# Kernel optimization log

Measured on AMD Instinct MI355X. Metric: run time of the kernel, lower is better.

## Reference

```python
import jax, jax.numpy as jnp
import numpy as np

NOISE_STD = 0.1
TOP_K = 2


def setup_inputs() -> dict:
    key = jax.random.key(0)
    k_x, k_n, k_w, k_keys = jax.random.split(key, 4)
    N, D_IN, D_Q, K = 16384, 2048, 256, 64
    x = jax.random.normal(k_x, (N, D_IN), dtype=jnp.float32)
    noise = jax.random.normal(k_n, (N, K), dtype=jnp.float32)
    # Linear params (kaiming-uniform-ish scale) and xavier-uniform keys
    w_q = jax.random.normal(k_w, (D_IN, D_Q), dtype=jnp.float32) * (1.0 / np.sqrt(D_IN))
    b_q = jnp.zeros((D_Q,), dtype=jnp.float32)
    lim = np.sqrt(6.0 / (K + D_Q))
    keys = jax.random.uniform(k_keys, (K, D_Q), dtype=jnp.float32, minval=-lim, maxval=lim)
    return {"x": x, "noise": noise, "w_q": w_q, "b_q": b_q, "keys": keys}


def reference(x, noise, w_q, b_q, keys):
    # query projection: [N, D_in] @ [D_in, D_q] -> [N, D_q]
    query = x @ w_q + b_q
    d_q = query.shape[-1]
    # router logits: [N, K], scaled dot product with expert keys
    logits = (query @ keys.T) * (1.0 / jnp.sqrt(jnp.asarray(d_q, query.dtype)))
    logits = logits + noise * NOISE_STD  # training-mode gating noise
    # top-k selection + softmax over selected logits only
    top_logits, top_idx = jax.lax.top_k(logits, TOP_K)       # [N, top_k]
    top_probs = jax.nn.softmax(top_logits, axis=-1)           # [N, top_k]
    # scatter selected probs into dense [N, K] gating tensor (zeros elsewhere)
    rows = jnp.arange(logits.shape[0])[:, None]               # [N, 1]
    gating_probs = jnp.zeros_like(logits).at[rows, top_idx].set(top_probs)
    return gating_probs, top_idx
```

## Files before the change

kernel.cpp:

```cpp
#include <hip/hip_runtime.h>

#define MROWS 16384
#define KD 2048
#define NQ 256
#define NE 64
#define INV_SQRT_DQ 0.0625f
#define NOISE_STD_C 0.1f

typedef _Float16 f16x8 __attribute__((ext_vector_type(8)));
typedef float f32x4 __attribute__((ext_vector_type(4)));

__device__ inline void split8v(f32x4 a, f32x4 b, f16x8* h, f16x8* l) {
    f16x8 hh, ll;
#pragma unroll
    for (int i = 0; i < 4; ++i) {
        _Float16 s = (_Float16)a[i];
        hh[i] = s; ll[i] = (_Float16)(a[i] - (float)s);
    }
#pragma unroll
    for (int i = 0; i < 4; ++i) {
        _Float16 s = (_Float16)b[i];
        hh[4 + i] = s; ll[4 + i] = (_Float16)(b[i] - (float)s);
    }
    *h = hh; *l = ll;
}

__global__ __launch_bounds__(256) void prep_w2(
    const float* __restrict__ w, const float* __restrict__ keys,
    const float* __restrict__ bq, _Float16* __restrict__ whp,
    _Float16* __restrict__ wlp, float* __restrict__ css) {
    const int tid = blockIdx.x * 256 + threadIdx.x;
    const int e = tid & 63;
    const int o = tid >> 6;
    const float* kp = keys + (size_t)e * NQ;
    const float* wp = w + (size_t)o * 8 * NQ;
    double acc[8];
#pragma unroll
    for (int j = 0; j < 8; ++j) acc[j] = 0.0;
    for (int q = 0; q < NQ; q += 4) {
        f32x4 kv = *(const f32x4*)(kp + q);
#pragma unroll
        for (int j = 0; j < 8; ++j) {
            f32x4 wv = *(const f32x4*)(wp + (size_t)j * NQ + q);
#pragma unroll
            for (int u = 0; u < 4; ++u)
                acc[j] += (double)wv[u] * (double)kv[u];
        }
    }
    const int kc32 = o >> 2;
    const int qqp  = o & 3;
    const size_t base = ((size_t)kc32 * 4 + (e >> 4)) * 512 + (size_t)(qqp * 16 + (e & 15)) * 8;
    f16x8 h, l;
#pragma unroll
    for (int j = 0; j < 8; ++j) {
        float v = (float)acc[j];
        _Float16 s = (_Float16)v;
        h[j] = s;
        l[j] = (_Float16)(v - (float)s);
    }
    *(f16x8*)(whp + base) = h;
    *(f16x8*)(wlp + base) = l;
    if (blockIdx.x == 0 && threadIdx.x < NE) {
        const float* kp2 = keys + (size_t)threadIdx.x * NQ;
        double s = 0.0;
        for (int q = 0; q < NQ; ++q) s += (double)bq[q] * (double)kp2[q];
        css[threadIdx.x] = (float)(s * 0.0625);
    }
}

__global__ __launch_bounds__(512) void gemm2_fused(
    const float* __restrict__ x, const _Float16* __restrict__ whp,
    const _Float16* __restrict__ wlp, const float* __restrict__ css,
    const float* __restrict__ noise, float* __restrict__ gate,
    float* __restrict__ idxout) {
    __shared__ __align__(16) char smem[65536];

    const int t = threadIdx.x;
    const int lane = t & 63;
    const int wv = t >> 6;
    const int wn = wv & 3;
    const int wm = wv >> 2;
    const int m0 = blockIdx.x * 64;
    const int f = lane & 15;
    const int qq = lane >> 4;

    const int srow = t >> 4;
    const int soct = t & 15;
    const int swoff = (soct ^ (srow & 7)) * 8;
    const f32x4* xq0 = (const f32x4*)(x + (size_t)(m0 + srow) * KD + soct * 8);
    const f32x4* xq1 = (const f32x4*)(x + (size_t)(m0 + srow + 32) * KD + soct * 8);

    const _Float16* bph = whp + (size_t)wn * 512 + lane * 8;
    const _Float16* bpl = wlp + (size_t)wn * 512 + lane * 8;

    f32x4 acc[2];
    acc[0] = {0.f, 0.f, 0.f, 0.f};
    acc[1] = {0.f, 0.f, 0.f, 0.f};

    f32x4 a0 = __builtin_nontemporal_load(xq0);
    f32x4 a1 = __builtin_nontemporal_load(xq0 + 1);
    f32x4 b0 = __builtin_nontemporal_load(xq1);
    f32x4 b1 = __builtin_nontemporal_load(xq1 + 1);
    {
        _Float16* Ah = (_Float16*)smem;
        _Float16* Al = Ah + 8192;
        f16x8 h8, l8;
        split8v(a0, a1, &h8, &l8);
        *(f16x8*)(Ah + srow * 128 + swoff) = h8;
        *(f16x8*)(Al + srow * 128 + swoff) = l8;
        split8v(b0, b1, &h8, &l8);
        *(f16x8*)(Ah + (srow + 32) * 128 + swoff) = h8;
        *(f16x8*)(Al + (srow + 32) * 128 + swoff) = l8;
    }
    a0 = __builtin_nontemporal_load(xq0 + 32);
    a1 = __builtin_nontemporal_load(xq0 + 33);
    b0 = __builtin_nontemporal_load(xq1 + 32);
    b1 = __builtin_nontemporal_load(xq1 + 33);
    __syncthreads();

    f16x8 bhS[4], blS[4];
#pragma unroll
    for (int ks = 0; ks < 4; ++ks) {
        bhS[ks] = *(const f16x8*)(bph + (size_t)ks * 2048);
        blS[ks] = *(const f16x8*)(bpl + (size_t)ks * 2048);
    }

    for (int i = 0; i < 16; ++i) {
        _Float16* AhC = (_Float16*)smem + (i & 1) * 16384;
        _Float16* AlC = AhC + 8192;
        _Float16* AhN = (_Float16*)smem + ((i & 1) ^ 1) * 16384;
        _Float16* AlN = AhN + 8192;

        if (i < 15) {
            f16x8 h8, l8;
            split8v(a0, a1, &h8, &l8);
            *(f16x8*)(AhN + srow * 128 + swoff) = h8;
            *(f16x8*)(AlN + srow * 128 + swoff) = l8;
            split8v(b0, b1, &h8, &l8);
            *(f16x8*)(AhN + (srow + 32) * 128 + swoff) = h8;
            *(f16x8*)(AlN + (srow + 32) * 128 + swoff) = l8;
        }
        if (i < 14) {
            a0 = __builtin_nontemporal_load(xq0 + (i + 2) * 32);
            a1 = __builtin_nontemporal_load(xq0 + (i + 2) * 32 + 1);
            b0 = __builtin_nontemporal_load(xq1 + (i + 2) * 32);
            b1 = __builtin_nontemporal_load(xq1 + (i + 2) * 32 + 1);
        }
#pragma unroll
        for (int ks = 0; ks < 4; ++ks) {
            f16x8 ah[2], al[2];
#pragma unroll
            for (int mt = 0; mt < 2; ++mt) {
                const int row = (wm * 2 + mt) * 16 + f;
                const int ab = row * 128 + (((ks * 4 + qq) ^ (row & 7)) * 8);
                ah[mt] = *(const f16x8*)(AhC + ab);
                al[mt] = *(const f16x8*)(AlC + ab);
            }
#pragma unroll
            for (int mt = 0; mt < 2; ++mt) {
                acc[mt] = __builtin_amdgcn_mfma_f32_16x16x32_f16(ah[mt], bhS[ks], acc[mt], 0, 0, 0);
                acc[mt] = __builtin_amdgcn_mfma_f32_16x16x32_f16(ah[mt], blS[ks], acc[mt], 0, 0, 0);
                acc[mt] = __builtin_amdgcn_mfma_f32_16x16x32_f16(al[mt], bhS[ks], acc[mt], 0, 0, 0);
            }
            int gn = i * 4 + ks + 4;
            if (gn > 63) gn = 63;
            bhS[ks] = *(const f16x8*)(bph + (size_t)gn * 2048);
            blS[ks] = *(const f16x8*)(bpl + (size_t)gn * 2048);
        }
        asm volatile("" ::: "memory");
        __builtin_amdgcn_s_waitcnt(0xC07F);
        __builtin_amdgcn_s_barrier();
        asm volatile("" ::: "memory");
    }

    float* LG = (float*)smem;
    const int e = wn * 16 + f;
    const float cse = css[e];
#pragma unroll
    for (int mt = 0; mt < 2; ++mt)
#pragma unroll
        for (int r = 0; r < 4; ++r) {
            int row = (wm * 2 + mt) * 16 + qq * 4 + r;
            LG[row * 65 + e] = acc[mt][r] * INV_SQRT_DQ + cse +
                               NOISE_STD_C * noise[(size_t)(m0 + row) * NE + e];
        }
    __syncthreads();

    for (int i = 0; i < 8; ++i) {
        int r = wv * 8 + i;
        float v = LG[r * 65 + lane];
        float v1 = v; int i1 = lane;
#pragma unroll
        for (int off = 32; off; off >>= 1) {
            float ov = __shfl_xor(v1, off);
            int oi = __shfl_xor(i1, off);
            if (ov > v1 || (ov == v1 && oi < i1)) { v1 = ov; i1 = oi; }
        }
        float v2 = (lane == i1) ? -1e30f : v;
        int i2 = lane;
#pragma unroll
        for (int off = 32; off; off >>= 1) {
            float ov = __shfl_xor(v2, off);
            int oi = __shfl_xor(i2, off);
            if (ov > v2 || (ov == v2 && oi < i2)) { v2 = ov; i2 = oi; }
        }
        float ex = expf(v2 - v1);
        float p1 = 1.0f / (1.0f + ex);
        float p2 = ex * p1;
        float g = (lane == i1) ? p1 : ((lane == i2) ? p2 : 0.0f);
        gate[(size_t)(m0 + r) * NE + lane] = g;
        if (lane == 0) {
            float2 ii = make_float2((float)i1, (float)i2);
            *(float2*)(idxout + (size_t)(m0 + r) * 2) = ii;
        }
    }
}

extern "C" void kernel_launch(void* const* d_in, const int* in_sizes, int n_in,
                              void* d_out, int out_size, void* d_ws, size_t ws_size,
                              hipStream_t stream) {
    const float* x     = (const float*)d_in[0];
    const float* noise = (const float*)d_in[1];
    const float* w_q   = (const float*)d_in[2];
    const float* b_q   = (const float*)d_in[3];
    const float* keys  = (const float*)d_in[4];
    float* out = (float*)d_out;

    char* ws = (char*)d_ws;
    _Float16* whp = (_Float16*)ws;
    _Float16* wlp = (_Float16*)(ws + (256u << 10));
    float* css    = (float*)(ws + (512u << 10));

    prep_w2<<<64, 256, 0, stream>>>(w_q, keys, b_q, whp, wlp, css);
    gemm2_fused<<<256, 512, 0, stream>>>(x, whp, wlp, css, noise,
                                         out, out + (size_t)MROWS * NE);
}
```

Baseline: 252.4 us.

## Split-K GEMM with 16-row blocks and register-direct x loads, parallelize prep

The main kernel moves from 64-row tiles staged through double-buffered LDS to 16-row blocks. Each of 4 waves handles a quarter of K, loads x straight into registers, and a wave-0 reduction through shared memory combines the partial sums. This drops the per-iteration LDS staging and barriers and raises the grid from 256 to 1024 blocks at 2 blocks per CU. The prep kernel also splits its dot products across 4 threads with a shared-memory reduction, so it can run on more blocks. In exchange, each wave now fetches the full fused weight matrix instead of sharing it, which raises L2 traffic for the weights.

```diff
diff --git a/kernel.cpp b/kernel.cpp
--- a/kernel.cpp
+++ b/kernel.cpp
@@ -29,15 +29,17 @@
     const float* __restrict__ w, const float* __restrict__ keys,
     const float* __restrict__ bq, _Float16* __restrict__ whp,
     _Float16* __restrict__ wlp, float* __restrict__ css) {
-    const int tid = blockIdx.x * 256 + threadIdx.x;
-    const int e = tid & 63;
-    const int o = tid >> 6;
-    const float* kp = keys + (size_t)e * NQ;
-    const float* wp = w + (size_t)o * 8 * NQ;
+    __shared__ double part[4][64][8];
+    const int t = threadIdx.x;
+    const int e = t & 63;
+    const int qc = t >> 6;
+    const int o = blockIdx.x;
+    const float* kp = keys + (size_t)e * NQ + qc * 64;
+    const float* wp = w + (size_t)o * 8 * NQ + qc * 64;
     double acc[8];
 #pragma unroll
     for (int j = 0; j < 8; ++j) acc[j] = 0.0;
-    for (int q = 0; q < NQ; q += 4) {
+    for (int q = 0; q < 64; q += 4) {
         f32x4 kv = *(const f32x4*)(kp + q);
 #pragma unroll
         for (int j = 0; j < 8; ++j) {
@@ -47,147 +49,144 @@
                 acc[j] += (double)wv[u] * (double)kv[u];
         }
     }
-    const int kc32 = o >> 2;
-    const int qqp  = o & 3;
-    const size_t base = ((size_t)kc32 * 4 + (e >> 4)) * 512 + (size_t)(qqp * 16 + (e & 15)) * 8;
-    f16x8 h, l;
-#pragma unroll
-    for (int j = 0; j < 8; ++j) {
-        float v = (float)acc[j];
-        _Float16 s = (_Float16)v;
-        h[j] = s;
-        l[j] = (_Float16)(v - (float)s);
-    }
-    *(f16x8*)(whp + base) = h;
-    *(f16x8*)(wlp + base) = l;
-    if (blockIdx.x == 0 && threadIdx.x < NE) {
-        const float* kp2 = keys + (size_t)threadIdx.x * NQ;
-        double s = 0.0;
-        for (int q = 0; q < NQ; ++q) s += (double)bq[q] * (double)kp2[q];
-        css[threadIdx.x] = (float)(s * 0.0625);
-    }
-}
-
-__global__ __launch_bounds__(512) void gemm2_fused(
+#pragma unroll
+    for (int j = 0; j < 8; ++j) part[qc][e][j] = acc[j];
+    __syncthreads();
+    if (t < 64) {
+        const size_t base = ((size_t)(o >> 2) * 4 + (e >> 4)) * 512 +
+                            (size_t)((o & 3) * 16 + (e & 15)) * 8;
+        f16x8 h, l;
+#pragma unroll
+        for (int j = 0; j < 8; ++j) {
+            float v = (float)(part[0][e][j] + part[1][e][j] +
+                              part[2][e][j] + part[3][e][j]);
+            _Float16 s = (_Float16)v;
+            h[j] = s;
+            l[j] = (_Float16)(v - (float)s);
+        }
+        *(f16x8*)(whp + base) = h;
+        *(f16x8*)(wlp + base) = l;
+    }
+    if (blockIdx.x == 0) {
+        __syncthreads();
+        double p = 0.0;
+        const float* bp2 = bq + qc * 64;
+        const float* kp2 = keys + (size_t)e * NQ + qc * 64;
+        for (int q = 0; q < 64; q += 4) {
+            f32x4 bv = *(const f32x4*)(bp2 + q);
+            f32x4 kv = *(const f32x4*)(kp2 + q);
+#pragma unroll
+            for (int u = 0; u < 4; ++u)
+                p += (double)bv[u] * (double)kv[u];
+        }
+        part[qc][e][0] = p;
+        __syncthreads();
+        if (t < 64)
+            css[e] = (float)((part[0][e][0] + part[1][e][0] +
+                              part[2][e][0] + part[3][e][0]) * 0.0625);
+    }
+}
+
+__global__ __launch_bounds__(256, 2) void gemm3_fused(
     const float* __restrict__ x, const _Float16* __restrict__ whp,
     const _Float16* __restrict__ wlp, const float* __restrict__ css,
     const float* __restrict__ noise, float* __restrict__ gate,
     float* __restrict__ idxout) {
-    __shared__ __align__(16) char smem[65536];
+    __shared__ float comb[3 * 1040];
+    __shared__ float LG[16 * 65];
 
     const int t = threadIdx.x;
     const int lane = t & 63;
     const int wv = t >> 6;
-    const int wn = wv & 3;
-    const int wm = wv >> 2;
-    const int m0 = blockIdx.x * 64;
+    const int m0 = blockIdx.x * 16;
     const int f = lane & 15;
     const int qq = lane >> 4;
 
-    const int srow = t >> 4;
-    const int soct = t & 15;
-    const int swoff = (soct ^ (srow & 7)) * 8;
-    const f32x4* xq0 = (const f32x4*)(x + (size_t)(m0 + srow) * KD + soct * 8);
-    const f32x4* xq1 = (const f32x4*)(x + (size_t)(m0 + srow + 32) * KD + soct * 8);
-
-    const _Float16* bph = whp + (size_t)wn * 512 + lane * 8;
-    const _Float16* bpl = wlp + (size_t)wn * 512 + lane * 8;
-
-    f32x4 acc[2];
-    acc[0] = {0.f, 0.f, 0.f, 0.f};
-    acc[1] = {0.f, 0.f, 0.f, 0.f};
-
-    f32x4 a0 = __builtin_nontemporal_load(xq0);
-    f32x4 a1 = __builtin_nontemporal_load(xq0 + 1);
-    f32x4 b0 = __builtin_nontemporal_load(xq1);
-    f32x4 b1 = __builtin_nontemporal_load(xq1 + 1);
-    {
-        _Float16* Ah = (_Float16*)smem;
-        _Float16* Al = Ah + 8192;
-        f16x8 h8, l8;
-        split8v(a0, a1, &h8, &l8);
-        *(f16x8*)(Ah + srow * 128 + swoff) = h8;
-        *(f16x8*)(Al + srow * 128 + swoff) = l8;
-        split8v(b0, b1, &h8, &l8);
-        *(f16x8*)(Ah + (srow + 32) * 128 + swoff) = h8;
-        *(f16x8*)(Al + (srow + 32) * 128 + swoff) = l8;
-    }
-    a0 = __builtin_nontemporal_load(xq0 + 32);
-    a1 = __builtin_nontemporal_load(xq0 + 33);
-    b0 = __builtin_nontemporal_load(xq1 + 32);
-    b1 = __builtin_nontemporal_load(xq1 + 33);
+    const float* xp = x + (size_t)(m0 + f) * KD + wv * 512 + qq * 8;
+    const _Float16* bph = whp + (size_t)(wv * 16) * 2048 + lane * 8;
+    const _Float16* bpl = wlp + (size_t)(wv * 16) * 2048 + lane * 8;
+
+    f32x4 acc[4];
+#pragma unroll
+    for (int nt = 0; nt < 4; ++nt) acc[nt] = {0.f, 0.f, 0.f, 0.f};
+
+    f32x4 xb[4][2];
+    f16x8 bhS[2][4], blS[2][4];
+
+#pragma unroll
+    for (int s = 0; s < 4; ++s) {
+        const f32x4* p = (const f32x4*)(xp + s * 32);
+        xb[s][0] = __builtin_nontemporal_load(p);
+        xb[s][1] = __builtin_nontemporal_load(p + 1);
+    }
+#pragma unroll
+    for (int s = 0; s < 2; ++s)
+#pragma unroll
+        for (int nt = 0; nt < 4; ++nt) {
+            bhS[s][nt] = *(const f16x8*)(bph + ((size_t)s * 4 + nt) * 512);
+            blS[s][nt] = *(const f16x8*)(bpl + ((size_t)s * 4 + nt) * 512);
+        }
+
+#pragma unroll
+    for (int s = 0; s < 16; ++s) {
+        const int js = s & 3;
+        const int c = s & 1;
+        f16x8 ah, al;
+        split8v(xb[js][0], xb[js][1], &ah, &al);
+#pragma unroll
+        for (int nt = 0; nt < 4; ++nt) {
+            acc[nt] = __builtin_amdgcn_mfma_f32_16x16x32_f16(ah, bhS[c][nt], acc[nt], 0, 0, 0);
+            acc[nt] = __builtin_amdgcn_mfma_f32_16x16x32_f16(ah, blS[c][nt], acc[nt], 0, 0, 0);
+            acc[nt] = __builtin_amdgcn_mfma_f32_16x16x32_f16(al, bhS[c][nt], acc[nt], 0, 0, 0);
+        }
+        if (s < 12) {
+            const f32x4* p = (const f32x4*)(xp + (s + 4) * 32);
+            xb[js][0] = __builtin_nontemporal_load(p);
+            xb[js][1] = __builtin_nontemporal_load(p + 1);
+        }
+        if (s < 14) {
+#pragma unroll
+            for (int nt = 0; nt < 4; ++nt) {
+                bhS[c][nt] = *(const f16x8*)(bph + ((size_t)(s + 2) * 4 + nt) * 512);
+                blS[c][nt] = *(const f16x8*)(bpl + ((size_t)(s + 2) * 4 + nt) * 512);
+            }
+        }
+    }
+
+    if (wv > 0) {
+#pragma unroll
+        for (int nt = 0; nt < 4; ++nt)
+#pragma unroll
+            for (int r = 0; r < 4; ++r)
+                comb[(wv - 1) * 1040 + (nt * 4 + r) * 65 + lane] = acc[nt][r];
+    }
     __syncthreads();
-
-    f16x8 bhS[4], blS[4];
-#pragma unroll
-    for (int ks = 0; ks < 4; ++ks) {
-        bhS[ks] = *(const f16x8*)(bph + (size_t)ks * 2048);
-        blS[ks] = *(const f16x8*)(bpl + (size_t)ks * 2048);
-    }
-
-    for (int i = 0; i < 16; ++i) {
-        _Float16* AhC = (_Float16*)smem + (i & 1) * 16384;
-        _Float16* AlC = AhC + 8192;
-        _Float16* AhN = (_Float16*)smem + ((i & 1) ^ 1) * 16384;
-        _Float16* AlN = AhN + 8192;
-
-        if (i < 15) {
-            f16x8 h8, l8;
-            split8v(a0, a1, &h8, &l8);
-            *(f16x8*)(AhN + srow * 128 + swoff) = h8;
-            *(f16x8*)(AlN + srow * 128 + swoff) = l8;
-            split8v(b0, b1, &h8, &l8);
-            *(f16x8*)(AhN + (srow + 32) * 128 + swoff) = h8;
-            *(f16x8*)(AlN + (srow + 32) * 128 + swoff) = l8;
-        }
-        if (i < 14) {
-            a0 = __builtin_nontemporal_load(xq0 + (i + 2) * 32);
-            a1 = __builtin_nontemporal_load(xq0 + (i + 2) * 32 + 1);
-            b0 = __builtin_nontemporal_load(xq1 + (i + 2) * 32);
-            b1 = __builtin_nontemporal_load(xq1 + (i + 2) * 32 + 1);
-        }
-#pragma unroll
-        for (int ks = 0; ks < 4; ++ks) {
-            f16x8 ah[2], al[2];
-#pragma unroll
-            for (int mt = 0; mt < 2; ++mt) {
-                const int row = (wm * 2 + mt) * 16 + f;
-                const int ab = row * 128 + (((ks * 4 + qq) ^ (row & 7)) * 8);
-                ah[mt] = *(const f16x8*)(AhC + ab);
-                al[mt] = *(const f16x8*)(AlC + ab);
+    if (wv == 0) {
+#pragma unroll
+        for (int nt = 0; nt < 4; ++nt)
+#pragma unroll
+            for (int r = 0; r < 4; ++r) {
+                const int idx = (nt * 4 + r) * 65 + lane;
+                acc[nt][r] += comb[idx];
+                acc[nt][r] += comb[1040 + idx];
+                acc[nt][r] += comb[2080 + idx];
             }
 #pragma unroll
-            for (int mt = 0; mt < 2; ++mt) {
-                acc[mt] = __builtin_amdgcn_mfma_f32_16x16x32_f16(ah[mt], bhS[ks], acc[mt], 0, 0, 0);
-                acc[mt] = __builtin_amdgcn_mfma_f32_16x16x32_f16(ah[mt], blS[ks], acc[mt], 0, 0, 0);
-                acc[mt] = __builtin_amdgcn_mfma_f32_16x16x32_f16(al[mt], bhS[ks], acc[mt], 0, 0, 0);
+        for (int nt = 0; nt < 4; ++nt) {
+            const int e = nt * 16 + f;
+            const float cs = css[e];
+#pragma unroll
+            for (int r = 0; r < 4; ++r) {
+                const int row = qq * 4 + r;
+                LG[row * 65 + e] = acc[nt][r] * INV_SQRT_DQ + cs +
+                                   NOISE_STD_C * noise[(size_t)(m0 + row) * NE + e];
             }
-            int gn = i * 4 + ks + 4;
-            if (gn > 63) gn = 63;
-            bhS[ks] = *(const f16x8*)(bph + (size_t)gn * 2048);
-            blS[ks] = *(const f16x8*)(bpl + (size_t)gn * 2048);
-        }
-        asm volatile("" ::: "memory");
-        __builtin_amdgcn_s_waitcnt(0xC07F);
-        __builtin_amdgcn_s_barrier();
-        asm volatile("" ::: "memory");
-    }
-
-    float* LG = (float*)smem;
-    const int e = wn * 16 + f;
-    const float cse = css[e];
-#pragma unroll
-    for (int mt = 0; mt < 2; ++mt)
-#pragma unroll
-        for (int r = 0; r < 4; ++r) {
-            int row = (wm * 2 + mt) * 16 + qq * 4 + r;
-            LG[row * 65 + e] = acc[mt][r] * INV_SQRT_DQ + cse +
-                               NOISE_STD_C * noise[(size_t)(m0 + row) * NE + e];
-        }
+        }
+    }
     __syncthreads();
 
-    for (int i = 0; i < 8; ++i) {
-        int r = wv * 8 + i;
+    for (int i = 0; i < 4; ++i) {
+        const int r = wv * 4 + i;
         float v = LG[r * 65 + lane];
         float v1 = v; int i1 = lane;
 #pragma unroll
@@ -231,7 +230,7 @@
     _Float16* wlp = (_Float16*)(ws + (256u << 10));
     float* css    = (float*)(ws + (512u << 10));
 
-    prep_w2<<<64, 256, 0, stream>>>(w_q, keys, b_q, whp, wlp, css);
-    gemm2_fused<<<256, 512, 0, stream>>>(x, whp, wlp, css, noise,
-                                         out, out + (size_t)MROWS * NE);
-}
+    prep_w2<<<256, 256, 0, stream>>>(w_q, keys, b_q, whp, wlp, css);
+    gemm3_fused<<<1024, 256, 0, stream>>>(x, whp, wlp, css, noise,
+                                          out, out + (size_t)MROWS * NE);
+}
```

After: 236.5 us. -6.3%, faster.
